# Kernel tuning notes

Measured on AMD Instinct MI355X. Metric: run time of the kernel, lower is better.

Reference implementation:

```python
import jax, jax.numpy as jnp
import numpy as np

N_NODES = 100000
N_EDGES = 1600000
F_IN = 128
HIDDEN = [128, 128]
F_OUT = 64


def _glorot(key, shape):
    fan_in, fan_out = shape[1], shape[0]
    lim = jnp.sqrt(6.0 / (fan_in + fan_out))
    return jax.random.uniform(key, shape, jnp.float32, -lim, lim)


def setup_inputs() -> dict:
    key = jax.random.key(0)
    ks = jax.random.split(key, 12)
    x = jax.random.normal(ks[0], (N_NODES, F_IN), jnp.float32)
    edge_index = jax.random.randint(ks[1], (2, N_EDGES), 0, N_NODES, jnp.int64)
    dims = [F_IN] + HIDDEN + [F_OUT]  # [128, 128, 128, 64]
    inp = {"x": x, "edge_index": edge_index}
    for i in range(3):
        din, dout = dims[i], dims[i + 1]
        inp[f"Wl{i}"] = _glorot(ks[2 + 3 * i], (dout, din))  # neighbor lin (lin_l)
        inp[f"Wr{i}"] = _glorot(ks[3 + 3 * i], (dout, din))  # root lin (lin_r)
        inp[f"b{i}"] = jnp.zeros((dout,), jnp.float32)
    return inp


def sage_conv(x, src, dst, Wl, Wr, b):
    # PyG SAGEConv, aggr='mean': out = lin_l(mean_{j in N(i)} x_j) + lin_r(x_i) + bias
    msg = x[src]  # [E, Fin] gather from source nodes
    agg = jax.ops.segment_sum(msg, dst, num_segments=N_NODES)  # [N, Fin]
    deg = jax.ops.segment_sum(jnp.ones((src.shape[0],), x.dtype), dst,
                              num_segments=N_NODES)  # [N]
    mean = agg / jnp.maximum(deg, 1.0)[:, None]
    return mean @ Wl.T + x @ Wr.T + b


def reference(x, edge_index, Wl0, Wr0, b0, Wl1, Wr1, b1, Wl2, Wr2, b2):
    src, dst = edge_index[0], edge_index[1]
    h = jax.nn.relu(sage_conv(x, src, dst, Wl0, Wr0, b0))
    h = jax.nn.relu(sage_conv(h, src, dst, Wl1, Wr1, b1))
    out = sage_conv(h, src, dst, Wl2, Wr2, b2)  # final_conv: no relu
    return out
```

## Files before the change

kernel.cpp:

```cpp
#include <hip/hip_runtime.h>

#define NF 128
#define CHUNK 4096

typedef __attribute__((ext_vector_type(8))) short bf16x8;
typedef __attribute__((ext_vector_type(4))) float f32x4;
typedef __attribute__((ext_vector_type(2))) float f32x2;

__device__ __forceinline__ unsigned short f2b(float f) {
    unsigned int u = __float_as_uint(f);
    unsigned int r = (u + 0x7fffu + ((u >> 16) & 1u)) >> 16;
    return (unsigned short)r;
}

__device__ __forceinline__ void gld_lds16(const void* g, const void* l) {
    __builtin_amdgcn_global_load_lds(
        (const __attribute__((address_space(1))) unsigned int*)(unsigned long long)g,
        (__attribute__((address_space(3))) unsigned int*)(unsigned int)(unsigned long long)l,
        16, 0, 0);
}


__global__ __launch_bounds__(256) void prep_kernel(
        const float* __restrict__ x, unsigned short* __restrict__ xb, int n4,
        const float* __restrict__ Wl0, const float* __restrict__ Wr0, unsigned short* __restrict__ Wc0,
        const float* __restrict__ Wl1, const float* __restrict__ Wr1, unsigned short* __restrict__ Wc1,
        const float* __restrict__ Wl2, const float* __restrict__ Wr2, const float* __restrict__ b2,
        unsigned short* __restrict__ Wst, float* __restrict__ bst,
        const int* __restrict__ dst, int* __restrict__ hist, int E, int NB,
        int bCvt, int bW0, int bW1, int bWs) {
    __shared__ int hsh[512];
    const int blk = blockIdx.x;
    const int tid = threadIdx.x;
    if (blk < bCvt) {
        int i = blk * 256 + tid;
        if (i < n4) {
            float4 v = *(const float4*)&x[(size_t)i * 4];
            uint2 o;
            o.x = (unsigned int)f2b(v.x) | ((unsigned int)f2b(v.y) << 16);
            o.y = (unsigned int)f2b(v.z) | ((unsigned int)f2b(v.w) << 16);
            *(uint2*)&xb[(size_t)i * 4] = o;
        }
    } else if (blk < bW1) {
        const bool first = blk < bW0;
        int i = (blk - (first ? bCvt : bW0)) * 256 + tid;
        const float* Wl = first ? Wl0 : Wl1;
        const float* Wr = first ? Wr0 : Wr1;
        unsigned short* Wc = first ? Wc0 : Wc1;
        int f = i >> 7, k = i & 127;
        Wc[f * 256 + k] = f2b(Wl[i]);
        Wc[f * 256 + 128 + k] = f2b(Wr[i]);
    } else if (blk < bWs) {
        int i = (blk - bW1) * 256 + tid;
        int f = i >> 7, k = i & 127;
        Wst[f * 128 + k] = f2b(Wl2[i]);
        Wst[(f + 64) * 128 + k] = f2b(Wr2[i]);
        if (k == 0) {
            bst[f] = 0.f;
            bst[f + 64] = b2[f];
        }
    } else {
        const int hb = blk - bWs;
        for (int i = tid; i < NB; i += 256) hsh[i] = 0;
        __syncthreads();
        const int e0 = hb * CHUNK;
        for (int i = tid; i < CHUNK; i += 256) {
            int e = e0 + i;
            if (e < E) atomicAdd(&hsh[dst[e] >> 8], 1);
        }
        __syncthreads();
        for (int i = tid; i < NB; i += 256) hist[hb * NB + i] = hsh[i];
    }
}


__global__ __launch_bounds__(256) void sb_sum(const int* __restrict__ hist,
                                              int* __restrict__ bsum,
                                              int T, int NB, int NBLK) {
    int i = blockIdx.x * 256 + threadIdx.x;
    int v = 0;
    if (i < T) {
        int b = i / NBLK, blk = i - b * NBLK;
        v = hist[blk * NB + b];
    }
#pragma unroll
    for (int d = 32; d; d >>= 1) v += __shfl_down(v, d, 64);
    __shared__ int wsum[4];
    if ((threadIdx.x & 63) == 0) wsum[threadIdx.x >> 6] = v;
    __syncthreads();
    if (threadIdx.x == 0) bsum[blockIdx.x] = wsum[0] + wsum[1] + wsum[2] + wsum[3];
}

__global__ __launch_bounds__(1024) void sb_scan(const int* __restrict__ bsum,
                                                int* __restrict__ bpre, int NS) {
    __shared__ int s[1024];
    int t = threadIdx.x;
    int v = (t < NS) ? bsum[t] : 0;
    s[t] = v;
    __syncthreads();
    for (int d = 1; d < 1024; d <<= 1) {
        int u = (t >= d) ? s[t - d] : 0;
        __syncthreads();
        s[t] += u;
        __syncthreads();
    }
    if (t < NS) bpre[t] = s[t] - v;
}

__global__ __launch_bounds__(256) void sb_apply(const int* __restrict__ hist,
                                                const int* __restrict__ bpre,
                                                int* __restrict__ base,
                                                int* __restrict__ bstart,
                                                int T, int NB, int NBLK, int E) {
    __shared__ int s[256];
    int i = blockIdx.x * 256 + threadIdx.x;
    int t = threadIdx.x;
    int v = 0;
    int b = 0, blk = 0;
    if (i < T) {
        b = i / NBLK;
        blk = i - b * NBLK;
        v = hist[blk * NB + b];
    }
    s[t] = v;
    __syncthreads();
    for (int d = 1; d < 256; d <<= 1) {
        int u = (t >= d) ? s[t - d] : 0;
        __syncthreads();
        s[t] += u;
        __syncthreads();
    }
    if (i < T) {
        int val = bpre[blockIdx.x] + s[t] - v;
        base[i] = val;
        if (blk == 0) bstart[b] = val;
        if (i == 0) bstart[NB] = E;
    }
}

__global__ __launch_bounds__(256) void scat_kernel(const int* __restrict__ src,
                                                   const int* __restrict__ dst,
                                                   const int* __restrict__ base,
                                                   unsigned int* __restrict__ recs,
                                                   int E, int NB, int NBLK) {
    __shared__ int cur[512];
    const int blk = blockIdx.x;
    for (int b = threadIdx.x; b < NB; b += 256) cur[b] = base[b * NBLK + blk];
    __syncthreads();
    const int e0 = blk * CHUNK;
    for (int i = threadIdx.x; i < CHUNK; i += 256) {
        int e = e0 + i;
        if (e >= E) continue;
        int d = dst[e];
        int b = d >> 8;
        int pos = atomicAdd(&cur[b], 1);
        recs[pos] = (unsigned int)src[e] | ((unsigned int)(d & 255) << 24);
    }
}

__global__ __launch_bounds__(256) void csr_kernel(const unsigned int* __restrict__ recs,
                                                  const int* __restrict__ bstart,
                                                  int* __restrict__ offs,
                                                  float* __restrict__ rdeg,
                                                  int* __restrict__ csr,
                                                  int N, int E) {
    __shared__ int cnt[256];
    __shared__ int sc[256];
    __shared__ int cur[256];
    const int b = blockIdx.x;
    const int t = threadIdx.x;
    const int s0 = bstart[b], s1 = bstart[b + 1];
    cnt[t] = 0;
    __syncthreads();
    for (int i = s0 + t; i < s1; i += 256) atomicAdd(&cnt[recs[i] >> 24], 1);
    __syncthreads();
    int v = cnt[t];
    sc[t] = v;
    __syncthreads();
    for (int d = 1; d < 256; d <<= 1) {
        int u = (t >= d) ? sc[t - d] : 0;
        __syncthreads();
        sc[t] += u;
        __syncthreads();
    }
    int excl = sc[t] - v;
    int node = b * 256 + t;
    if (node < N) {
        offs[node] = s0 + excl;
        rdeg[node] = 1.0f / (float)(v > 1 ? v : 1);
        if (node == N - 1) offs[N] = E;
    }
    cur[t] = s0 + excl;
    __syncthreads();
    for (int i = s0 + t; i < s1; i += 256) {
        unsigned int r = recs[i];
        int pos = atomicAdd(&cur[r >> 24], 1);
        csr[pos] = (int)(r & 0xFFFFFFu);
    }
}


__global__ __launch_bounds__(256) void agg_kernel(
        const unsigned short* __restrict__ h, const int* __restrict__ offs,
        const int* __restrict__ csr, const float* __restrict__ rdeg,
        unsigned short* __restrict__ meanout, int N) {
    const int node = blockIdx.x * 4 + (threadIdx.x >> 6);
    const int lane = threadIdx.x & 63;
    if (node >= N) return;
    const int s0 = offs[node], s1 = offs[node + 1];
    const char* __restrict__ hb = (const char*)h;
    const unsigned lane4 = (unsigned)lane * 4u;
    f32x2 acc = {0.f, 0.f};
    for (int base = s0; base < s1; base += 64) {
        const int cnt = min(64, s1 - base);
        const int boff = csr[base + min(lane, cnt - 1)] << 8;
        for (int j = 0; j < cnt; j += 16) {
            if (j + 16 <= cnt) {
                unsigned o[16];
#pragma unroll
                for (int k = 0; k < 16; ++k)
                    o[k] = (unsigned)__shfl(boff, j + k, 64) + lane4;
                unsigned int v[16];
#pragma unroll
                for (int k = 0; k < 16; ++k)
                    v[k] = *(const unsigned int*)(hb + o[k]);
#pragma unroll
                for (int k = 0; k < 16; ++k)
                    acc += (f32x2){__uint_as_float(v[k] << 16),
                                   __uint_as_float(v[k] & 0xffff0000u)};
            } else {
                unsigned o[16];
#pragma unroll
                for (int k = 0; k < 16; ++k)
                    o[k] = (unsigned)__shfl(boff, min(j + k, cnt - 1), 64) + lane4;
                unsigned int v[16];
#pragma unroll
                for (int k = 0; k < 16; ++k)
                    v[k] = *(const unsigned int*)(hb + o[k]);
#pragma unroll
                for (int k = 0; k < 16; ++k)
                    if (j + k < cnt)
                        acc += (f32x2){__uint_as_float(v[k] << 16),
                                       __uint_as_float(v[k] & 0xffff0000u)};
            }
        }
    }
    float r = rdeg[node];
    unsigned int o = (unsigned int)f2b(acc.x * r) | ((unsigned int)f2b(acc.y * r) << 16);
    *(unsigned int*)&meanout[(size_t)node * NF + lane * 2] = o;
}


__global__ __launch_bounds__(256) void agg2_kernel(
        const unsigned short* __restrict__ z, const int* __restrict__ offs,
        const int* __restrict__ csr, const float* __restrict__ rdeg,
        float* __restrict__ out, int N) {
    const int node = blockIdx.x * 4 + (threadIdx.x >> 6);
    const int lane = threadIdx.x & 63;
    if (node >= N) return;
    const int hlf = lane >> 5;
    const int fl  = lane & 31;
    const int s0 = offs[node], s1 = offs[node + 1];
    const char* __restrict__ zb = (const char*)z;
    const unsigned fl4 = (unsigned)fl * 4u;
    f32x2 acc = {0.f, 0.f};
    for (int base = s0; base < s1; base += 64) {
        const int cnt = min(64, s1 - base);
        const int boff = csr[base + min(lane, cnt - 1)] << 8;
        for (int j = 0; j < cnt; j += 16) {
            if (j + 16 <= cnt) {
                unsigned o[8];
#pragma unroll
                for (int k = 0; k < 8; ++k)
                    o[k] = (unsigned)__shfl(boff, j + 2 * k + hlf, 64) + fl4;
                unsigned int v[8];
#pragma unroll
                for (int k = 0; k < 8; ++k)
                    v[k] = *(const unsigned int*)(zb + o[k]);
#pragma unroll
                for (int k = 0; k < 8; ++k)
                    acc += (f32x2){__uint_as_float(v[k] << 16),
                                   __uint_as_float(v[k] & 0xffff0000u)};
            } else {
                unsigned o[8];
#pragma unroll
                for (int k = 0; k < 8; ++k)
                    o[k] = (unsigned)__shfl(boff, min(j + 2 * k + hlf, cnt - 1), 64) + fl4;
                unsigned int v[8];
#pragma unroll
                for (int k = 0; k < 8; ++k)
                    v[k] = *(const unsigned int*)(zb + o[k]);
#pragma unroll
                for (int k = 0; k < 8; ++k)
                    if (j + 2 * k + hlf < cnt)
                        acc += (f32x2){__uint_as_float(v[k] << 16),
                                       __uint_as_float(v[k] & 0xffff0000u)};
            }
        }
    }
    acc.x += __shfl_xor(acc.x, 32, 64);
    acc.y += __shfl_xor(acc.y, 32, 64);
    if (hlf == 0) {
        float r = rdeg[node];
        unsigned int vr = *(const unsigned int*)(zb + (size_t)node * 256 + 128 + fl * 4);
        float2 o;
        o.x = acc.x * r + __uint_as_float(vr << 16);
        o.y = acc.y * r + __uint_as_float(vr & 0xffff0000u);
        *(float2*)&out[(size_t)node * 64 + fl * 2] = o;
    }
}


template <int FOUT, bool RELU>
__global__ __launch_bounds__(256) void gemm_kernel(
        const unsigned short* __restrict__ Abuf,
        const unsigned short* __restrict__ Hbuf,
        const unsigned short* __restrict__ Wcat,
        const float* __restrict__ bias,
        unsigned short* __restrict__ outb,
        int N) {
    __shared__ unsigned short As[128 * 256];

    const int tid = threadIdx.x, wid = tid >> 6, lane = tid & 63;
    const int m0 = blockIdx.x * 128;
    char* Ac = (char*)As;
    const char* Ab = (const char*)Abuf;
    const char* Hb = (const char*)Hbuf;
    const char* Wb = (const char*)Wcat;

#pragma unroll
    for (int i = 0; i < 16; ++i) {
        int off = wid * 16384 + i * 1024 + lane * 16;
        int row = off >> 9, c = off & 511;
        int c2 = c ^ ((row & 7) << 4);
        const char* srcp = (c2 < 256) ? (Ab + (size_t)(m0 + row) * 256 + c2)
                                      : (Hb + (size_t)(m0 + row) * 256 + (c2 - 256));
        gld_lds16(srcp, Ac + wid * 16384 + i * 1024);
    }
    asm volatile("s_waitcnt vmcnt(0)" ::: "memory");
    __syncthreads();

    constexpr int MI = (FOUT == 128) ? 4 : 2;
    constexpr int NI = 4;
    const int lm = lane & 15, ko = lane >> 4;
    const int wmBase = (FOUT == 128) ? (wid >> 1) * 64 : wid * 32;
    const int wnBase = (FOUT == 128) ? (wid & 1) * 64 : 0;

    f32x4 acc[MI][NI];
#pragma unroll
    for (int i = 0; i < MI; ++i)
#pragma unroll
        for (int j = 0; j < NI; ++j)
            acc[i][j] = (f32x4){0.f, 0.f, 0.f, 0.f};

#pragma unroll
    for (int ks = 0; ks < 8; ++ks) {
        const int kb = ks * 64 + ko * 16;
        bf16x8 a[MI], b[NI];
#pragma unroll
        for (int j = 0; j < NI; ++j) {
            int row = wnBase + j * 16 + lm;
            b[j] = *(const bf16x8*)(Wb + row * 512 + kb);
        }
#pragma unroll
        for (int i = 0; i < MI; ++i) {
            int row = wmBase + i * 16 + lm;
            a[i] = *(const bf16x8*)(Ac + row * 512 + (kb ^ ((row & 7) << 4)));
        }
#pragma unroll
        for (int i = 0; i < MI; ++i)
#pragma unroll
            for (int j = 0; j < NI; ++j)
                acc[i][j] = __builtin_amdgcn_mfma_f32_16x16x32_bf16(b[j], a[i], acc[i][j], 0, 0, 0);
    }

#pragma unroll
    for (int i = 0; i < MI; ++i) {
        const int node = m0 + wmBase + i * 16 + lm;
        if (node < N) {
#pragma unroll
            for (int j = 0; j < NI; ++j) {
                const int col0 = wnBase + j * 16 + ko * 4;
                const float4 bv = *(const float4*)&bias[col0];
                float v0 = acc[i][j][0] + bv.x;
                float v1 = acc[i][j][1] + bv.y;
                float v2 = acc[i][j][2] + bv.z;
                float v3 = acc[i][j][3] + bv.w;
                if (RELU) {
                    v0 = fmaxf(v0, 0.f); v1 = fmaxf(v1, 0.f);
                    v2 = fmaxf(v2, 0.f); v3 = fmaxf(v3, 0.f);
                }
                uint2 o;
                o.x = (unsigned int)f2b(v0) | ((unsigned int)f2b(v1) << 16);
                o.y = (unsigned int)f2b(v2) | ((unsigned int)f2b(v3) << 16);
                *(uint2*)&outb[(size_t)node * FOUT + col0] = o;
            }
        }
    }
}


__global__ __launch_bounds__(256) void gemmz_kernel(
        const unsigned short* __restrict__ A,
        const unsigned short* __restrict__ W,
        const float* __restrict__ bias,
        unsigned short* __restrict__ outb,
        int N) {
    __shared__ unsigned short As[128 * 128];

    const int tid = threadIdx.x, wid = tid >> 6, lane = tid & 63;
    const int m0 = blockIdx.x * 128;
    char* Ac = (char*)As;
    const char* Ab = (const char*)A;
    const char* Wb = (const char*)W;

#pragma unroll
    for (int i = 0; i < 8; ++i) {
        int off = wid * 8192 + i * 1024 + lane * 16;
        int row = off >> 8, c = off & 255;
        int c2 = c ^ ((row & 7) << 4);
        gld_lds16(Ab + (size_t)(m0 + row) * 256 + c2, Ac + wid * 8192 + i * 1024);
    }
    asm volatile("s_waitcnt vmcnt(0)" ::: "memory");
    __syncthreads();

    const int lm = lane & 15, ko = lane >> 4;
    const int wmBase = (wid >> 1) * 64;
    const int wnBase = (wid & 1) * 64;

    f32x4 acc[4][4];
#pragma unroll
    for (int i = 0; i < 4; ++i)
#pragma unroll
        for (int j = 0; j < 4; ++j)
            acc[i][j] = (f32x4){0.f, 0.f, 0.f, 0.f};

#pragma unroll
    for (int ks = 0; ks < 4; ++ks) {
        const int kb = ks * 64 + ko * 16;
        bf16x8 a[4], b[4];
#pragma unroll
        for (int j = 0; j < 4; ++j) {
            int row = wnBase + j * 16 + lm;
            b[j] = *(const bf16x8*)(Wb + row * 256 + kb);
        }
#pragma unroll
        for (int i = 0; i < 4; ++i) {
            int row = wmBase + i * 16 + lm;
            a[i] = *(const bf16x8*)(Ac + row * 256 + (kb ^ ((row & 7) << 4)));
        }
#pragma unroll
        for (int i = 0; i < 4; ++i)
#pragma unroll
            for (int j = 0; j < 4; ++j)
                acc[i][j] = __builtin_amdgcn_mfma_f32_16x16x32_bf16(b[j], a[i], acc[i][j], 0, 0, 0);
    }

#pragma unroll
    for (int i = 0; i < 4; ++i) {
        const int node = m0 + wmBase + i * 16 + lm;
        if (node < N) {
#pragma unroll
            for (int j = 0; j < 4; ++j) {
                const int col0 = wnBase + j * 16 + ko * 4;
                const float4 bv = *(const float4*)&bias[col0];
                uint2 o;
                o.x = (unsigned int)f2b(acc[i][j][0] + bv.x) |
                      ((unsigned int)f2b(acc[i][j][1] + bv.y) << 16);
                o.y = (unsigned int)f2b(acc[i][j][2] + bv.z) |
                      ((unsigned int)f2b(acc[i][j][3] + bv.w) << 16);
                *(uint2*)&outb[(size_t)node * 128 + col0] = o;
            }
        }
    }
}


extern "C" void kernel_launch(void* const* d_in, const int* in_sizes, int n_in,
                              void* d_out, int out_size, void* d_ws, size_t ws_size,
                              hipStream_t stream) {
    const float* x   = (const float*)d_in[0];
    const int*   ei  = (const int*)d_in[1];
    const float* Wl0 = (const float*)d_in[2];
    const float* Wr0 = (const float*)d_in[3];
    const float* b0  = (const float*)d_in[4];
    const float* Wl1 = (const float*)d_in[5];
    const float* Wr1 = (const float*)d_in[6];
    const float* b1  = (const float*)d_in[7];
    const float* Wl2 = (const float*)d_in[8];
    const float* Wr2 = (const float*)d_in[9];
    const float* b2  = (const float*)d_in[10];
    float* out = (float*)d_out;

    const int N = in_sizes[0] / NF;
    const int E = in_sizes[1] / 2;
    const int* srcv = ei;
    const int* dstv = ei + E;

    const int NB   = (N + 255) >> 8;
    const int NBLK = (E + CHUNK - 1) / CHUNK;
    const int T    = NB * NBLK;
    const int NS   = (T + 255) / 256;

    char* w = (char*)d_ws;
    auto alloc = [&](size_t bytes) {
        void* p = (void*)w;
        w += (bytes + 255) & ~(size_t)255;
        return p;
    };
    unsigned short* xb   = (unsigned short*)alloc((size_t)N * NF * 2);
    unsigned short* h1b  = (unsigned short*)alloc((size_t)N * NF * 2);
    unsigned short* h2b  = (unsigned short*)alloc((size_t)N * NF * 2);
    unsigned short* mb   = (unsigned short*)alloc((size_t)N * NF * 2);
    unsigned short* z2b  = (unsigned short*)alloc((size_t)N * NF * 2);
    unsigned short* Wc0  = (unsigned short*)alloc((size_t)128 * 256 * 2);
    unsigned short* Wc1  = (unsigned short*)alloc((size_t)128 * 256 * 2);
    unsigned short* Wst2 = (unsigned short*)alloc((size_t)128 * 128 * 2);
    float*          bst2 = (float*)alloc((size_t)128 * 4);
    int*   offs   = (int*)alloc((size_t)(N + 1) * 4);
    int*   csr    = (int*)alloc((size_t)E * 4);
    float* rdeg   = (float*)alloc((size_t)N * 4);
    unsigned int* recs = (unsigned int*)alloc((size_t)E * 4);
    int*   hist   = (int*)alloc((size_t)T * 4);
    int*   base   = (int*)alloc((size_t)T * 4);
    int*   bstart = (int*)alloc((size_t)(NB + 1) * 4);
    int*   sb1    = (int*)alloc((size_t)1024 * 4);
    int*   sb2    = (int*)alloc((size_t)1024 * 4);

    const int n4 = N * NF / 4;
    const int bCvt = (n4 + 255) / 256;
    const int bW0  = bCvt + 64;
    const int bW1  = bW0 + 64;
    const int bWs  = bW1 + 32;
    const int bTot = bWs + NBLK;

    prep_kernel<<<bTot, 256, 0, stream>>>(x, xb, n4,
                                          Wl0, Wr0, Wc0, Wl1, Wr1, Wc1,
                                          Wl2, Wr2, b2, Wst2, bst2,
                                          dstv, hist, E, NB,
                                          bCvt, bW0, bW1, bWs);
    sb_sum<<<NS, 256, 0, stream>>>(hist, sb1, T, NB, NBLK);
    sb_scan<<<1, 1024, 0, stream>>>(sb1, sb2, NS);
    sb_apply<<<NS, 256, 0, stream>>>(hist, sb2, base, bstart, T, NB, NBLK, E);
    scat_kernel<<<NBLK, 256, 0, stream>>>(srcv, dstv, base, recs, E, NB, NBLK);
    csr_kernel<<<NB, 256, 0, stream>>>(recs, bstart, offs, rdeg, csr, N, E);

    const int ab = (N + 3) / 4;
    const int gb = (N + 127) / 128;

    agg_kernel<<<ab, 256, 0, stream>>>(xb, offs, csr, rdeg, mb, N);
    gemm_kernel<128, true><<<gb, 256, 0, stream>>>(mb, xb, Wc0, b0, h1b, N);

    agg_kernel<<<ab, 256, 0, stream>>>(h1b, offs, csr, rdeg, mb, N);
    gemm_kernel<128, true><<<gb, 256, 0, stream>>>(mb, h1b, Wc1, b1, h2b, N);

    gemmz_kernel<<<gb, 256, 0, stream>>>(h2b, Wst2, bst2, z2b, N);
    agg2_kernel<<<ab, 256, 0, stream>>>(z2b, offs, csr, rdeg, out, N);
}
```

Baseline: 302.5 us.

## Gather neighbor features in FP8 for the first two mean aggregations

Adds FP8 copies of the input features (written in the prep kernel) and of the layer-1 hidden output (via a new conversion kernel). The first two aggregation kernels now gather 1-byte values instead of bf16, halving random-gather traffic over the edges. This costs an extra conversion pass and buffer aliasing, and loses accuracy because FP8 e4m3 has only three mantissa bits. The histogram chunk size is also doubled.

Result: no change. 298.0 us (-1.5%).

```diff
diff --git a/kernel.cpp b/kernel.cpp
--- a/kernel.cpp
+++ b/kernel.cpp
@@ -1,7 +1,7 @@
 #include <hip/hip_runtime.h>
 
 #define NF 128
-#define CHUNK 4096
+#define CHUNK 8192
 
 typedef __attribute__((ext_vector_type(8))) short bf16x8;
 typedef __attribute__((ext_vector_type(4))) float f32x4;
@@ -22,7 +22,8 @@
 
 
 __global__ __launch_bounds__(256) void prep_kernel(
-        const float* __restrict__ x, unsigned short* __restrict__ xb, int n4,
+        const float* __restrict__ x, unsigned short* __restrict__ xb,
+        unsigned char* __restrict__ x8, int n4,
         const float* __restrict__ Wl0, const float* __restrict__ Wr0, unsigned short* __restrict__ Wc0,
         const float* __restrict__ Wl1, const float* __restrict__ Wr1, unsigned short* __restrict__ Wc1,
         const float* __restrict__ Wl2, const float* __restrict__ Wr2, const float* __restrict__ b2,
@@ -40,6 +41,9 @@
             o.x = (unsigned int)f2b(v.x) | ((unsigned int)f2b(v.y) << 16);
             o.y = (unsigned int)f2b(v.z) | ((unsigned int)f2b(v.w) << 16);
             *(uint2*)&xb[(size_t)i * 4] = o;
+            unsigned p = __builtin_amdgcn_cvt_pk_fp8_f32(v.x, v.y, 0, false);
+            p = __builtin_amdgcn_cvt_pk_fp8_f32(v.z, v.w, p, true);
+            *(unsigned int*)&x8[(size_t)i * 4] = p;
         }
     } else if (blk < bW1) {
         const bool first = blk < bW0;
@@ -74,6 +78,24 @@
 }
 
 
+__global__ __launch_bounds__(256) void cvt8_kernel(const unsigned short* __restrict__ in,
+                                                   unsigned char* __restrict__ out8, int n8) {
+    int i = blockIdx.x * 256 + threadIdx.x;
+    if (i >= n8) return;
+    uint4 v = *(const uint4*)&in[(size_t)i * 8];
+    float f0 = __uint_as_float(v.x << 16), f1 = __uint_as_float(v.x & 0xffff0000u);
+    float f2 = __uint_as_float(v.y << 16), f3 = __uint_as_float(v.y & 0xffff0000u);
+    float f4 = __uint_as_float(v.z << 16), f5 = __uint_as_float(v.z & 0xffff0000u);
+    float f6 = __uint_as_float(v.w << 16), f7 = __uint_as_float(v.w & 0xffff0000u);
+    unsigned lo = __builtin_amdgcn_cvt_pk_fp8_f32(f0, f1, 0, false);
+    lo = __builtin_amdgcn_cvt_pk_fp8_f32(f2, f3, lo, true);
+    unsigned hi = __builtin_amdgcn_cvt_pk_fp8_f32(f4, f5, 0, false);
+    hi = __builtin_amdgcn_cvt_pk_fp8_f32(f6, f7, hi, true);
+    uint2 o = make_uint2(lo, hi);
+    *(uint2*)&out8[(size_t)i * 8] = o;
+}
+
+
 __global__ __launch_bounds__(256) void sb_sum(const int* __restrict__ hist,
                                               int* __restrict__ bsum,
                                               int T, int NB, int NBLK) {
@@ -200,48 +222,50 @@
 }
 
 
-__global__ __launch_bounds__(256) void agg_kernel(
-        const unsigned short* __restrict__ h, const int* __restrict__ offs,
+__global__ __launch_bounds__(256) void agg8_kernel(
+        const unsigned char* __restrict__ h8, const int* __restrict__ offs,
         const int* __restrict__ csr, const float* __restrict__ rdeg,
         unsigned short* __restrict__ meanout, int N) {
     const int node = blockIdx.x * 4 + (threadIdx.x >> 6);
     const int lane = threadIdx.x & 63;
     if (node >= N) return;
     const int s0 = offs[node], s1 = offs[node + 1];
-    const char* __restrict__ hb = (const char*)h;
-    const unsigned lane4 = (unsigned)lane * 4u;
+    const char* __restrict__ hb = (const char*)h8;
+    const unsigned lane2 = (unsigned)lane * 2u;
     f32x2 acc = {0.f, 0.f};
     for (int base = s0; base < s1; base += 64) {
         const int cnt = min(64, s1 - base);
-        const int boff = csr[base + min(lane, cnt - 1)] << 8;
+        const int boff = csr[base + min(lane, cnt - 1)] << 7;
         for (int j = 0; j < cnt; j += 16) {
             if (j + 16 <= cnt) {
                 unsigned o[16];
 #pragma unroll
                 for (int k = 0; k < 16; ++k)
-                    o[k] = (unsigned)__shfl(boff, j + k, 64) + lane4;
+                    o[k] = (unsigned)__shfl(boff, j + k, 64) + lane2;
                 unsigned int v[16];
 #pragma unroll
                 for (int k = 0; k < 16; ++k)
-                    v[k] = *(const unsigned int*)(hb + o[k]);
-#pragma unroll
-                for (int k = 0; k < 16; ++k)
-                    acc += (f32x2){__uint_as_float(v[k] << 16),
-                                   __uint_as_float(v[k] & 0xffff0000u)};
+                    v[k] = *(const unsigned short*)(hb + o[k]);
+#pragma unroll
+                for (int k = 0; k < 16; ++k) {
+                    acc.x += __builtin_amdgcn_cvt_f32_fp8(v[k], 0);
+                    acc.y += __builtin_amdgcn_cvt_f32_fp8(v[k], 1);
+                }
             } else {
                 unsigned o[16];
 #pragma unroll
                 for (int k = 0; k < 16; ++k)
-                    o[k] = (unsigned)__shfl(boff, min(j + k, cnt - 1), 64) + lane4;
+                    o[k] = (unsigned)__shfl(boff, min(j + k, cnt - 1), 64) + lane2;
                 unsigned int v[16];
 #pragma unroll
                 for (int k = 0; k < 16; ++k)
-                    v[k] = *(const unsigned int*)(hb + o[k]);
+                    v[k] = *(const unsigned short*)(hb + o[k]);
 #pragma unroll
                 for (int k = 0; k < 16; ++k)
-                    if (j + k < cnt)
-                        acc += (f32x2){__uint_as_float(v[k] << 16),
-                                       __uint_as_float(v[k] & 0xffff0000u)};
+                    if (j + k < cnt) {
+                        acc.x += __builtin_amdgcn_cvt_f32_fp8(v[k], 0);
+                        acc.y += __builtin_amdgcn_cvt_f32_fp8(v[k], 1);
+                    }
             }
         }
     }
@@ -512,7 +536,10 @@
     unsigned short* h1b  = (unsigned short*)alloc((size_t)N * NF * 2);
     unsigned short* h2b  = (unsigned short*)alloc((size_t)N * NF * 2);
     unsigned short* mb   = (unsigned short*)alloc((size_t)N * NF * 2);
-    unsigned short* z2b  = (unsigned short*)alloc((size_t)N * NF * 2);
+    unsigned char*  u8   = (unsigned char*)alloc((size_t)N * NF * 2);
+    unsigned char*  x8   = u8;
+    unsigned char*  h18  = u8 + (size_t)N * NF;
+    unsigned short* z2b  = (unsigned short*)u8;
     unsigned short* Wc0  = (unsigned short*)alloc((size_t)128 * 256 * 2);
     unsigned short* Wc1  = (unsigned short*)alloc((size_t)128 * 256 * 2);
     unsigned short* Wst2 = (unsigned short*)alloc((size_t)128 * 128 * 2);
@@ -534,7 +561,7 @@
     const int bWs  = bW1 + 32;
     const int bTot = bWs + NBLK;
 
-    prep_kernel<<<bTot, 256, 0, stream>>>(x, xb, n4,
+    prep_kernel<<<bTot, 256, 0, stream>>>(x, xb, x8, n4,
                                           Wl0, Wr0, Wc0, Wl1, Wr1, Wc1,
                                           Wl2, Wr2, b2, Wst2, bst2,
                                           dstv, hist, E, NB,
@@ -547,11 +574,13 @@
 
     const int ab = (N + 3) / 4;
     const int gb = (N + 127) / 128;
-
-    agg_kernel<<<ab, 256, 0, stream>>>(xb, offs, csr, rdeg, mb, N);
+    const int n8 = N * NF / 8;
+
+    agg8_kernel<<<ab, 256, 0, stream>>>(x8, offs, csr, rdeg, mb, N);
     gemm_kernel<128, true><<<gb, 256, 0, stream>>>(mb, xb, Wc0, b0, h1b, N);
 
-    agg_kernel<<<ab, 256, 0, stream>>>(h1b, offs, csr, rdeg, mb, N);
+    cvt8_kernel<<<(n8 + 255) / 256, 256, 0, stream>>>(h1b, h18, n8);
+    agg8_kernel<<<ab, 256, 0, stream>>>(h18, offs, csr, rdeg, mb, N);
     gemm_kernel<128, true><<<gb, 256, 0, stream>>>(mb, h1b, Wc1, b1, h2b, N);
 
     gemmz_kernel<<<gb, 256, 0, stream>>>(h2b, Wst2, bst2, z2b, N);
```
